# Kernel tuning notes

Measured on AMD Instinct MI355X. Metric: run time of the kernel, lower is better.

The kernel has to match this reference:

```python
import jax, jax.numpy as jnp
import numpy as np

B, L, D = 2, 4096, 1024
H, HD = 16, D // 16
W = 256          # window_size
C = 256          # chunk/block size (== W, so each block sees prev + current block)
NC = L // C
SCALE = HD ** -0.5


def complex_linear(z, Wr, Wi):
    # z: [..., D, 2]; W*: [out, in] (torch Linear convention y = x @ W^T)
    xr, xi = z[..., 0], z[..., 1]
    yr = jnp.einsum('...i,oi->...o', xr, Wr) - jnp.einsum('...i,oi->...o', xi, Wi)
    yi = jnp.einsum('...i,oi->...o', xr, Wi) + jnp.einsum('...i,oi->...o', xi, Wr)
    return jnp.stack([yr, yi], axis=-1)


def _heads(x):
    # [B, L, D, 2] -> [B, H, NC, C, HD, 2]
    return x.reshape(B, L, H, HD, 2).transpose(0, 2, 1, 3, 4).reshape(B, H, NC, C, HD, 2)


def _band_mask():
    # block c, query local qi (global i = c*C + qi), key local kj over [prev block | cur block]
    # global j = (c-1)*C + kj ; valid iff 0 <= j <= i and i - j < W
    c = jnp.arange(NC)[:, None, None]
    qi = jnp.arange(C)[None, :, None]
    kj = jnp.arange(2 * C)[None, None, :]
    i = c * C + qi
    j = (c - 1) * C + kj
    return (j >= 0) & (j <= i) & (i - j < W)  # [NC, C, 2C]


def setup_inputs() -> dict:
    key = jax.random.key(0)
    ks = jax.random.split(key, 9)
    s = D ** -0.5
    inp = {'z': jax.random.normal(ks[0], (B, L, D, 2), jnp.float32)}
    names = ['Wq_r', 'Wq_i', 'Wk_r', 'Wk_i', 'Wv_r', 'Wv_i', 'Wo_r', 'Wo_i']
    for n, k in zip(names, ks[1:]):
        inp[n] = jax.random.normal(k, (D, D), jnp.float32) * s
    return inp


def reference(z, Wq_r, Wq_i, Wk_r, Wk_i, Wv_r, Wv_i, Wo_r, Wo_i):
    q = _heads(complex_linear(z, Wq_r, Wq_i))  # [B,H,NC,C,HD,2]
    k = _heads(complex_linear(z, Wk_r, Wk_i))
    v = _heads(complex_linear(z, Wv_r, Wv_i))

    def with_prev(x):  # [B,H,NC,C,HD,2] -> [B,H,NC,2C,HD,2] (prev block | cur block)
        prev = jnp.concatenate([jnp.zeros_like(x[:, :, :1]), x[:, :, :-1]], axis=2)
        return jnp.concatenate([prev, x], axis=3)

    kc = with_prev(k)
    vc = with_prev(v)

    # Re(q * conj(k)) = qr*kr + qi*ki
    scores = (jnp.einsum('bhncd,bhnkd->bhnck', q[..., 0], kc[..., 0])
              + jnp.einsum('bhncd,bhnkd->bhnck', q[..., 1], kc[..., 1])) * SCALE
    scores = jnp.where(_band_mask()[None, None], scores, -jnp.inf)
    w = jax.nn.softmax(scores, axis=-1)  # [B,H,NC,C,2C]

    out_r = jnp.einsum('bhnck,bhnkd->bhncd', w, vc[..., 0])
    out_i = jnp.einsum('bhnck,bhnkd->bhncd', w, vc[..., 1])
    out = jnp.stack([out_r, out_i], axis=-1)           # [B,H,NC,C,HD,2]
    out = out.reshape(B, H, L, HD, 2).transpose(0, 2, 1, 3, 4).reshape(B, L, D, 2)
    return complex_linear(out, Wo_r, Wo_i)
```

## Files before the change

### kernel.cpp

```cpp
#include <hip/hip_runtime.h>
#include <hip/hip_bf16.h>
#include <stdint.h>


typedef __attribute__((ext_vector_type(8))) short bf16x8;
typedef __attribute__((ext_vector_type(8))) unsigned short u16x8;
typedef __attribute__((ext_vector_type(4))) float f32x4;

#define PA_SCALE 0.125f
#define UNR _Pragma("unroll")

__device__ __forceinline__ unsigned short f2bf(float f) {
  unsigned int u = __builtin_bit_cast(unsigned int, f);
  u += 0x7fffu + ((u >> 16) & 1u);
  return (unsigned short)(u >> 16);
}

#define GLD16(gp, lp)                                          \
  __builtin_amdgcn_global_load_lds(                            \
      (const __attribute__((address_space(1))) void*)(gp),     \
      (__attribute__((address_space(3))) void*)(lp), 16, 0, 0)

__global__ __launch_bounds__(256) void pa_pack_A(const float* __restrict__ z,
                                                 unsigned short* __restrict__ A1) {
  int idx = (blockIdx.x * 256 + threadIdx.x) * 8;
  int m = idx >> 10, d = idx & 1023;
  const float2* zp = (const float2*)z + idx;
  u16x8 re, im;
  UNR for (int j = 0; j < 8; ++j) {
    float2 f = zp[j];
    re[j] = f2bf(f.x);
    im[j] = f2bf(f.y);
  }
  *(u16x8*)(A1 + (size_t)m * 2048 + d)        = re;
  *(u16x8*)(A1 + (size_t)m * 2048 + 1024 + d) = im;
}

__global__ __launch_bounds__(256) void pa_pack_B(
    const float* __restrict__ Wq_r, const float* __restrict__ Wq_i,
    const float* __restrict__ Wk_r, const float* __restrict__ Wk_i,
    const float* __restrict__ Wv_r, const float* __restrict__ Wv_i,
    const float* __restrict__ Wo_r, const float* __restrict__ Wo_i,
    unsigned short* __restrict__ Bp) {
  int idx = (blockIdx.x * 256 + threadIdx.x) * 8;
  int n = idx >> 10, d = idx & 1023;
  int proj = n >> 11, part = (n >> 10) & 1, o = n & 1023;
  const float* Wr; const float* Wi;
  if (proj == 0)      { Wr = Wq_r; Wi = Wq_i; }
  else if (proj == 1) { Wr = Wk_r; Wi = Wk_i; }
  else if (proj == 2) { Wr = Wv_r; Wi = Wv_i; }
  else                { Wr = Wo_r; Wi = Wo_i; }
  const float* pr = Wr + (size_t)o * 1024 + d;
  const float* pi = Wi + (size_t)o * 1024 + d;
  u16x8 lo, hi;
  UNR for (int j = 0; j < 8; ++j) {
    float r = pr[j], im = pi[j];
    if (part == 0) { lo[j] = f2bf(r);  hi[j] = f2bf(-im); }
    else           { lo[j] = f2bf(im); hi[j] = f2bf(r);  }
  }
  *(u16x8*)(Bp + (size_t)n * 2048 + d)        = lo;
  *(u16x8*)(Bp + (size_t)n * 2048 + 1024 + d) = hi;
}

#define BARR()                              \
  do {                                      \
    __builtin_amdgcn_s_barrier();           \
    __builtin_amdgcn_sched_barrier(0);      \
  } while (0)

#define READ_A(P, MH)                                                         \
  UNR for (int i = 0; i < 4; ++i)                                             \
    UNR for (int ks = 0; ks < 2; ++ks)                                        \
      af[i][ks] = *(const bf16x8*)&lds[P][MH][aoff + i * 1024 +               \
                                              ((ks * 32 + koff) ^ cxor)];

#define READ_B(P, NH, DST)                                                    \
  UNR for (int j = 0; j < 2; ++j)                                             \
    UNR for (int ks = 0; ks < 2; ++ks)                                        \
      DST[j][ks] = *(const bf16x8*)&lds[P][2 + (NH)][boff + j * 1024 +        \
                                                     ((ks * 32 + koff) ^ cxor)];

#define MFMA_Q(MB, NB, BF)                                                    \
  UNR for (int ks = 0; ks < 2; ++ks)                                          \
    UNR for (int i = 0; i < 4; ++i)                                           \
      UNR for (int j = 0; j < 2; ++j)                                         \
        acc[(MB) + i][(NB) + j] = __builtin_amdgcn_mfma_f32_16x16x32_bf16(    \
            af[i][ks], BF[j][ks], acc[(MB) + i][(NB) + j], 0, 0, 0);

#define TILE(P, T)                                                            \
  {                                                                           \
    READ_A(P, 0);                                                             \
    READ_B(P, 0, b0);                                                         \
    stageB(0, (T) + 1);                                                       \
    BARR();                                                                   \
    __builtin_amdgcn_s_setprio(1);                                            \
    MFMA_Q(0, 0, b0);                                                         \
    __builtin_amdgcn_s_setprio(0);                                            \
    BARR();                                                                   \
    READ_B(P, 1, b1);                                                         \
    stageA(0, (T) + 2);                                                       \
    BARR();                                                                   \
    __builtin_amdgcn_s_setprio(1);                                            \
    MFMA_Q(0, 2, b1);                                                         \
    __builtin_amdgcn_s_setprio(0);                                            \
    BARR();                                                                   \
    READ_A(P, 1);                                                             \
    stageB(1, (T) + 2);                                                       \
    BARR();                                                                   \
    __builtin_amdgcn_s_setprio(1);                                            \
    MFMA_Q(4, 2, b1);                                                         \
    __builtin_amdgcn_s_setprio(0);                                            \
    BARR();                                                                   \
    stageA(1, (T) + 2);                                                       \
    BARR();                                                                   \
    __builtin_amdgcn_s_setprio(1);                                            \
    MFMA_Q(4, 0, b0);                                                         \
    __builtin_amdgcn_s_setprio(0);                                            \
    asm volatile("s_waitcnt vmcnt(6)" ::: "memory");                          \
    __builtin_amdgcn_sched_barrier(0);                                        \
    BARR();                                                                   \
  }

template <int EPI>
__global__ __launch_bounds__(512, 2) void pa_gemm8(
    const unsigned short* __restrict__ A,
    const unsigned short* __restrict__ B,
    void* __restrict__ Cout, int K, int N) {
  __shared__ unsigned short lds[2][4][128 * 64];

  const int tid = threadIdx.x;
  const int lane = tid & 63, wid = tid >> 6;
  const int wm = wid >> 2, wn = wid & 3;
  const int lr = lane & 15, lh = lane >> 4;

  const int nwg = gridDim.x * gridDim.y;
  const int wg = blockIdx.y * gridDim.x + blockIdx.x;
  const int cpx = nwg >> 3;
  const int swz = (wg & 7) * cpx + (wg >> 3);
  const int bx = swz % gridDim.x, by = swz / gridDim.x;
  const int tm0 = by * 256, tn0 = bx * 256;

  const int NT = K >> 6;

  const int srow = lane >> 3;
  const int scolS = ((lane & 7) ^ srow) * 8;

  auto stageA = [&](int half, int ts) {
    int t = ts < NT ? ts : ts - NT;
    const unsigned short* g0 = A + (size_t)(tm0 + half * 128) * K + t * 64 + scolS;
    unsigned short* l0 = &lds[ts & 1][half][0];
    UNR for (int c = 0; c < 2; ++c) {
      int chunk = wid * 2 + c;
      GLD16(g0 + (size_t)(chunk * 8 + srow) * K, l0 + chunk * 512);
    }
  };
  auto stageB = [&](int half, int ts) {
    int t = ts < NT ? ts : ts - NT;
    const unsigned short* g0 = B + (size_t)(tn0 + half * 128) * K + t * 64 + scolS;
    unsigned short* l0 = &lds[ts & 1][2 + half][0];
    UNR for (int c = 0; c < 2; ++c) {
      int chunk = wid * 2 + c;
      GLD16(g0 + (size_t)(chunk * 8 + srow) * K, l0 + chunk * 512);
    }
  };

  const int aoff = (wm * 64 + lr) * 64;
  const int boff = (wn * 32 + lr) * 64;
  const int koff = lh * 8;
  const int cxor = (lr & 7) * 8;

  f32x4 acc[8][4];
  f32x4 zero4 = {0.f, 0.f, 0.f, 0.f};
  UNR for (int i = 0; i < 8; ++i)
    UNR for (int j = 0; j < 4; ++j) acc[i][j] = zero4;

  bf16x8 af[4][2], b0[2][2], b1[2][2];

  stageA(0, 0); stageB(0, 0); stageB(1, 0); stageA(1, 0);
  stageA(0, 1); stageB(1, 1); stageA(1, 1);
  asm volatile("s_waitcnt vmcnt(6)" ::: "memory");
  __builtin_amdgcn_sched_barrier(0);
  __builtin_amdgcn_s_barrier();
  __builtin_amdgcn_sched_barrier(0);

  for (int t = 0; t < NT; t += 2) {
    TILE(0, t);
    TILE(1, t + 1);
  }

  UNR for (int mh = 0; mh < 2; ++mh)
    UNR for (int i = 0; i < 4; ++i)
      UNR for (int nh = 0; nh < 2; ++nh)
        UNR for (int j = 0; j < 2; ++j)
          UNR for (int r = 0; r < 4; ++r) {
            int row = tm0 + mh * 128 + wm * 64 + i * 16 + lh * 4 + r;
            int col = tn0 + nh * 128 + wn * 32 + j * 16 + lr;
            float v = acc[mh * 4 + i][nh * 2 + j][r];
            if (EPI == 0) {
              ((unsigned short*)Cout)[(size_t)row * N + col] = f2bf(v);
            } else {
              int part = col >> 10, dd = col & 1023;
              ((float*)Cout)[((size_t)row * 1024 + dd) * 2 + part] = v;
            }
          }
}

__global__ __launch_bounds__(256) void pa_attn(const unsigned short* __restrict__ C1,
                                               unsigned short* __restrict__ A2) {
  __shared__ unsigned short Ks[2][64][72];
  __shared__ unsigned short Vts[2][64][72];
  __shared__ unsigned short Ps[4][16][72];

  int bid = blockIdx.x;
  int qq = bid & 3, nc = (bid >> 2) & 15, h = (bid >> 6) & 15, b = bid >> 10;
  int tid = threadIdx.x;
  int l = tid & 63, wv = tid >> 6;
  int lr = l & 15, lh = l >> 4;

  const int C1LD = 6144;
  const int rowB = b * 4096;
  const int colQr = h * 64,        colQi = 1024 + h * 64;
  const int colKr = 2048 + h * 64, colKi = 3072 + h * 64;
  const int colVr = 4096 + h * 64, colVi = 5120 + h * 64;
  const int q0 = qq * 64;
  const int qw = q0 + wv * 16;

  bf16x8 qfr[2], qfi[2];
  {
    const unsigned short* pr = C1 + (size_t)(rowB + nc * 256 + qw + lr) * C1LD + colQr;
    const unsigned short* pi = C1 + (size_t)(rowB + nc * 256 + qw + lr) * C1LD + colQi;
    qfr[0] = *(const bf16x8*)(pr + lh * 8);
    qfr[1] = *(const bf16x8*)(pr + 32 + lh * 8);
    qfi[0] = *(const bf16x8*)(pi + lh * 8);
    qfi[1] = *(const bf16x8*)(pi + 32 + lh * 8);
  }

  f32x4 zero4 = {0.f, 0.f, 0.f, 0.f};
  f32x4 sac[5][4];
#pragma unroll
  for (int c = 0; c < 5; ++c)
#pragma unroll
    for (int f = 0; f < 4; ++f) sac[c][f] = zero4;

#pragma unroll
  for (int c = 0; c < 5; ++c) {
    __syncthreads();
#pragma unroll
    for (int s = 0; s < 4; ++s) {
      int seg = s * 256 + tid;
      int arr = seg >> 9, row = (seg >> 3) & 63, sg = seg & 7;
      int kj = q0 + c * 64 + row;
      int tok = (nc - 1) * 256 + kj; if (tok < 0) tok = 0;
      const unsigned short* src =
          C1 + (size_t)(rowB + tok) * C1LD + (arr ? colKi : colKr) + sg * 8;
      *(bf16x8*)&Ks[arr][row][sg * 8] = *(const bf16x8*)src;
    }
    __syncthreads();
#pragma unroll
    for (int kk = 0; kk < 2; ++kk) {
#pragma unroll
      for (int f = 0; f < 4; ++f) {
        bf16x8 br = *(const bf16x8*)&Ks[0][f * 16 + lr][kk * 32 + lh * 8];
        bf16x8 bi = *(const bf16x8*)&Ks[1][f * 16 + lr][kk * 32 + lh * 8];
        sac[c][f] = __builtin_amdgcn_mfma_f32_16x16x32_bf16(qfr[kk], br, sac[c][f], 0, 0, 0);
        sac[c][f] = __builtin_amdgcn_mfma_f32_16x16x32_bf16(qfi[kk], bi, sac[c][f], 0, 0, 0);
      }
    }
  }

  float mx[4] = {-1e30f, -1e30f, -1e30f, -1e30f};
#pragma unroll
  for (int c = 0; c < 5; ++c)
#pragma unroll
    for (int f = 0; f < 4; ++f)
#pragma unroll
      for (int r = 0; r < 4; ++r) {
        int qi_ = qw + lh * 4 + r;
        int kj  = q0 + c * 64 + f * 16 + lr;
        bool valid = (kj > qi_) && (kj <= qi_ + 256) && (nc > 0 || kj >= 256);
        float s = valid ? sac[c][f][r] * PA_SCALE : -1e30f;
        sac[c][f][r] = s;
        mx[r] = fmaxf(mx[r], s);
      }
#pragma unroll
  for (int r = 0; r < 4; ++r)
#pragma unroll
    for (int d = 1; d < 16; d <<= 1) mx[r] = fmaxf(mx[r], __shfl_xor(mx[r], d));

  float sm[4] = {0.f, 0.f, 0.f, 0.f};
#pragma unroll
  for (int c = 0; c < 5; ++c)
#pragma unroll
    for (int f = 0; f < 4; ++f)
#pragma unroll
      for (int r = 0; r < 4; ++r) {
        float p = __expf(sac[c][f][r] - mx[r]);
        sac[c][f][r] = p;
        sm[r] += p;
      }
#pragma unroll
  for (int r = 0; r < 4; ++r)
#pragma unroll
    for (int d = 1; d < 16; d <<= 1) sm[r] += __shfl_xor(sm[r], d);
  float inv[4];
#pragma unroll
  for (int r = 0; r < 4; ++r) inv[r] = 1.0f / sm[r];

  f32x4 oac[2][4];
#pragma unroll
  for (int p = 0; p < 2; ++p)
#pragma unroll
    for (int f = 0; f < 4; ++f) oac[p][f] = zero4;

#pragma unroll
  for (int c = 0; c < 5; ++c) {
    __syncthreads();
#pragma unroll
    for (int s = 0; s < 4; ++s) {
      int seg = s * 256 + tid;
      int arr = seg >> 9, row = (seg >> 3) & 63, sg = seg & 7;
      int kj = q0 + c * 64 + row;
      int tok = (nc - 1) * 256 + kj; if (tok < 0) tok = 0;
      const unsigned short* src =
          C1 + (size_t)(rowB + tok) * C1LD + (arr ? colVi : colVr) + sg * 8;
      bf16x8 v = *(const bf16x8*)src;
#pragma unroll
      for (int j = 0; j < 8; ++j) Vts[arr][sg * 8 + j][row] = (unsigned short)v[j];
    }
#pragma unroll
    for (int f = 0; f < 4; ++f)
#pragma unroll
      for (int r = 0; r < 4; ++r)
        Ps[wv][lh * 4 + r][f * 16 + lr] = f2bf(sac[c][f][r]);
    __syncthreads();

    bf16x8 pa0 = *(const bf16x8*)&Ps[wv][lr][lh * 8];
    bf16x8 pa1 = *(const bf16x8*)&Ps[wv][lr][32 + lh * 8];
#pragma unroll
    for (int kk = 0; kk < 2; ++kk) {
      bf16x8 pak = kk ? pa1 : pa0;
#pragma unroll
      for (int fc = 0; fc < 4; ++fc) {
        bf16x8 vr = *(const bf16x8*)&Vts[0][fc * 16 + lr][kk * 32 + lh * 8];
        bf16x8 vi = *(const bf16x8*)&Vts[1][fc * 16 + lr][kk * 32 + lh * 8];
        oac[0][fc] = __builtin_amdgcn_mfma_f32_16x16x32_bf16(pak, vr, oac[0][fc], 0, 0, 0);
        oac[1][fc] = __builtin_amdgcn_mfma_f32_16x16x32_bf16(pak, vi, oac[1][fc], 0, 0, 0);
      }
    }
  }

#pragma unroll
  for (int fc = 0; fc < 4; ++fc)
#pragma unroll
    for (int r = 0; r < 4; ++r) {
      int m  = rowB + nc * 256 + qw + lh * 4 + r;
      int hd = fc * 16 + lr;
      A2[(size_t)m * 2048 + h * 64 + hd]        = f2bf(oac[0][fc][r] * inv[r]);
      A2[(size_t)m * 2048 + 1024 + h * 64 + hd] = f2bf(oac[1][fc][r] * inv[r]);
    }
}

extern "C" void kernel_launch(void* const* d_in, const int* in_sizes, int n_in,
                              void* d_out, int out_size, void* d_ws, size_t ws_size,
                              hipStream_t stream) {
  const float* z = (const float*)d_in[0];
  unsigned short* A1 = (unsigned short*)d_ws;
  unsigned short* Bp = (unsigned short*)((char*)d_ws + 33554432ull);
  unsigned short* C1 = (unsigned short*)((char*)d_ws + 67108864ull);
  float* out = (float*)d_out;

  pa_pack_A<<<4096, 256, 0, stream>>>(z, A1);
  pa_pack_B<<<4096, 256, 0, stream>>>(
      (const float*)d_in[1], (const float*)d_in[2],
      (const float*)d_in[3], (const float*)d_in[4],
      (const float*)d_in[5], (const float*)d_in[6],
      (const float*)d_in[7], (const float*)d_in[8], Bp);
  pa_gemm8<0><<<dim3(24, 32), 512, 0, stream>>>(A1, Bp, C1, 2048, 6144);
  pa_attn<<<2048, 256, 0, stream>>>(C1, A1);
  pa_gemm8<1><<<dim3(8, 32), 512, 0, stream>>>(A1, Bp + (size_t)6144 * 2048, out,
                                               2048, 2048);
}
```

Before: 384.8 us.

## Share K/V tiles across 128 queries per attention block with 8 waves

```diff
diff --git a/kernel.cpp b/kernel.cpp
--- a/kernel.cpp
+++ b/kernel.cpp
@@ -205,24 +205,58 @@
           }
 }
 
-__global__ __launch_bounds__(256) void pa_attn(const unsigned short* __restrict__ C1,
+#define QK1(SI)                                                               \
+  UNR for (int kk = 0; kk < 2; ++kk)                                          \
+    UNR for (int f = 0; f < 4; ++f) {                                         \
+      bf16x8 br = *(const bf16x8*)&Ks[0][f * 16 + lr][kk * 32 + lh * 8];      \
+      bf16x8 bi = *(const bf16x8*)&Ks[1][f * 16 + lr][kk * 32 + lh * 8];      \
+      sac[SI][f] = __builtin_amdgcn_mfma_f32_16x16x32_bf16(qfr[kk], br,       \
+                                                           sac[SI][f], 0, 0, 0); \
+      sac[SI][f] = __builtin_amdgcn_mfma_f32_16x16x32_bf16(qfi[kk], bi,       \
+                                                           sac[SI][f], 0, 0, 0); \
+    }
+
+#define PW1(SI)                                                               \
+  UNR for (int f = 0; f < 4; ++f)                                             \
+    UNR for (int r = 0; r < 4; ++r)                                           \
+      Ps[wv][lh * 4 + r][f * 16 + lr] = f2bf(sac[SI][f][r]);
+
+#define PV1()                                                                 \
+  {                                                                           \
+    bf16x8 pa0 = *(const bf16x8*)&Ps[wv][lr][lh * 8];                         \
+    bf16x8 pa1 = *(const bf16x8*)&Ps[wv][lr][32 + lh * 8];                    \
+    UNR for (int kk = 0; kk < 2; ++kk) {                                      \
+      bf16x8 pak = kk ? pa1 : pa0;                                            \
+      UNR for (int fc = 0; fc < 4; ++fc) {                                    \
+        bf16x8 vr = *(const bf16x8*)&Vts[0][fc * 16 + lr][kk * 32 + lh * 8];  \
+        bf16x8 vi = *(const bf16x8*)&Vts[1][fc * 16 + lr][kk * 32 + lh * 8];  \
+        oac[0][fc] = __builtin_amdgcn_mfma_f32_16x16x32_bf16(pak, vr,         \
+                                                             oac[0][fc], 0, 0, 0); \
+        oac[1][fc] = __builtin_amdgcn_mfma_f32_16x16x32_bf16(pak, vi,         \
+                                                             oac[1][fc], 0, 0, 0); \
+      }                                                                       \
+    }                                                                         \
+  }
+
+__global__ __launch_bounds__(512) void pa_attn(const unsigned short* __restrict__ C1,
                                                unsigned short* __restrict__ A2) {
   __shared__ unsigned short Ks[2][64][72];
   __shared__ unsigned short Vts[2][64][72];
-  __shared__ unsigned short Ps[4][16][72];
+  __shared__ unsigned short Ps[8][16][72];
 
   int bid = blockIdx.x;
-  int qq = bid & 3, nc = (bid >> 2) & 15, h = (bid >> 6) & 15, b = bid >> 10;
+  int half = bid & 1, nc = (bid >> 1) & 15, h = (bid >> 5) & 15, b = bid >> 9;
   int tid = threadIdx.x;
   int l = tid & 63, wv = tid >> 6;
   int lr = l & 15, lh = l >> 4;
+  int base = wv >> 2;
 
   const int C1LD = 6144;
   const int rowB = b * 4096;
   const int colQr = h * 64,        colQi = 1024 + h * 64;
   const int colKr = 2048 + h * 64, colKi = 3072 + h * 64;
   const int colVr = 4096 + h * 64, colVi = 5120 + h * 64;
-  const int q0 = qq * 64;
+  const int q0 = half * 128;
   const int qw = q0 + wv * 16;
 
   bf16x8 qfr[2], qfi[2];
@@ -243,11 +277,11 @@
     for (int f = 0; f < 4; ++f) sac[c][f] = zero4;
 
 #pragma unroll
-  for (int c = 0; c < 5; ++c) {
+  for (int c = 0; c < 6; ++c) {
     __syncthreads();
 #pragma unroll
-    for (int s = 0; s < 4; ++s) {
-      int seg = s * 256 + tid;
+    for (int s = 0; s < 2; ++s) {
+      int seg = s * 512 + tid;
       int arr = seg >> 9, row = (seg >> 3) & 63, sg = seg & 7;
       int kj = q0 + c * 64 + row;
       int tok = (nc - 1) * 256 + kj; if (tok < 0) tok = 0;
@@ -256,30 +290,22 @@
       *(bf16x8*)&Ks[arr][row][sg * 8] = *(const bf16x8*)src;
     }
     __syncthreads();
-#pragma unroll
-    for (int kk = 0; kk < 2; ++kk) {
-#pragma unroll
-      for (int f = 0; f < 4; ++f) {
-        bf16x8 br = *(const bf16x8*)&Ks[0][f * 16 + lr][kk * 32 + lh * 8];
-        bf16x8 bi = *(const bf16x8*)&Ks[1][f * 16 + lr][kk * 32 + lh * 8];
-        sac[c][f] = __builtin_amdgcn_mfma_f32_16x16x32_bf16(qfr[kk], br, sac[c][f], 0, 0, 0);
-        sac[c][f] = __builtin_amdgcn_mfma_f32_16x16x32_bf16(qfi[kk], bi, sac[c][f], 0, 0, 0);
-      }
-    }
+    if (wv < 4) { if (c < 5) { QK1(c); } }
+    else        { if (c >= 1) { QK1(c - 1); } }
   }
 
   float mx[4] = {-1e30f, -1e30f, -1e30f, -1e30f};
 #pragma unroll
-  for (int c = 0; c < 5; ++c)
+  for (int si = 0; si < 5; ++si)
 #pragma unroll
     for (int f = 0; f < 4; ++f)
 #pragma unroll
       for (int r = 0; r < 4; ++r) {
         int qi_ = qw + lh * 4 + r;
-        int kj  = q0 + c * 64 + f * 16 + lr;
+        int kj  = q0 + (si + base) * 64 + f * 16 + lr;
         bool valid = (kj > qi_) && (kj <= qi_ + 256) && (nc > 0 || kj >= 256);
-        float s = valid ? sac[c][f][r] * PA_SCALE : -1e30f;
-        sac[c][f][r] = s;
+        float s = valid ? sac[si][f][r] * PA_SCALE : -1e30f;
+        sac[si][f][r] = s;
         mx[r] = fmaxf(mx[r], s);
       }
 #pragma unroll
@@ -289,13 +315,13 @@
 
   float sm[4] = {0.f, 0.f, 0.f, 0.f};
 #pragma unroll
-  for (int c = 0; c < 5; ++c)
+  for (int si = 0; si < 5; ++si)
 #pragma unroll
     for (int f = 0; f < 4; ++f)
 #pragma unroll
       for (int r = 0; r < 4; ++r) {
-        float p = __expf(sac[c][f][r] - mx[r]);
-        sac[c][f][r] = p;
+        float p = __expf(sac[si][f][r] - mx[r]);
+        sac[si][f][r] = p;
         sm[r] += p;
       }
 #pragma unroll
@@ -313,11 +339,11 @@
     for (int f = 0; f < 4; ++f) oac[p][f] = zero4;
 
 #pragma unroll
-  for (int c = 0; c < 5; ++c) {
+  for (int c = 0; c < 6; ++c) {
     __syncthreads();
 #pragma unroll
-    for (int s = 0; s < 4; ++s) {
-      int seg = s * 256 + tid;
+    for (int s = 0; s < 2; ++s) {
+      int seg = s * 512 + tid;
       int arr = seg >> 9, row = (seg >> 3) & 63, sg = seg & 7;
       int kj = q0 + c * 64 + row;
       int tok = (nc - 1) * 256 + kj; if (tok < 0) tok = 0;
@@ -327,26 +353,11 @@
 #pragma unroll
       for (int j = 0; j < 8; ++j) Vts[arr][sg * 8 + j][row] = (unsigned short)v[j];
     }
-#pragma unroll
-    for (int f = 0; f < 4; ++f)
-#pragma unroll
-      for (int r = 0; r < 4; ++r)
-        Ps[wv][lh * 4 + r][f * 16 + lr] = f2bf(sac[c][f][r]);
+    if (wv < 4) { if (c < 5) { PW1(c); } }
+    else        { if (c >= 1) { PW1(c - 1); } }
     __syncthreads();
-
-    bf16x8 pa0 = *(const bf16x8*)&Ps[wv][lr][lh * 8];
-    bf16x8 pa1 = *(const bf16x8*)&Ps[wv][lr][32 + lh * 8];
-#pragma unroll
-    for (int kk = 0; kk < 2; ++kk) {
-      bf16x8 pak = kk ? pa1 : pa0;
-#pragma unroll
-      for (int fc = 0; fc < 4; ++fc) {
-        bf16x8 vr = *(const bf16x8*)&Vts[0][fc * 16 + lr][kk * 32 + lh * 8];
-        bf16x8 vi = *(const bf16x8*)&Vts[1][fc * 16 + lr][kk * 32 + lh * 8];
-        oac[0][fc] = __builtin_amdgcn_mfma_f32_16x16x32_bf16(pak, vr, oac[0][fc], 0, 0, 0);
-        oac[1][fc] = __builtin_amdgcn_mfma_f32_16x16x32_bf16(pak, vi, oac[1][fc], 0, 0, 0);
-      }
-    }
+    if (wv < 4) { if (c < 5) { PV1(); } }
+    else        { if (c >= 1) { PV1(); } }
   }
 
 #pragma unroll
@@ -376,7 +387,7 @@
       (const float*)d_in[5], (const float*)d_in[6],
       (const float*)d_in[7], (const float*)d_in[8], Bp);
   pa_gemm8<0><<<dim3(24, 32), 512, 0, stream>>>(A1, Bp, C1, 2048, 6144);
-  pa_attn<<<2048, 256, 0, stream>>>(C1, A1);
+  pa_attn<<<1024, 512, 0, stream>>>(C1, A1);
   pa_gemm8<1><<<dim3(8, 32), 512, 0, stream>>>(A1, Bp + (size_t)6144 * 2048, out,
                                                2048, 2048);
 }
```

After: 384.2 us. Within noise of the previous version (-0.2%).
